# Performance work log

Measured on AMD Instinct MI355X. Metric: run time of the kernel, lower is better.

## Reference

```python
import jax, jax.numpy as jnp
import numpy as np

DIM = 1024
GROUP = 16
N_LIN = 18   # 6 blocks * 3 quantized linears
N_LN = 5
RANK = 32
BATCH = 32768


def _dequant(q, s):
    # q: [DIM, DIM] int values in [0,16); s: [DIM*DIM/GROUP] per-group scales
    w = (q.reshape(-1, GROUP).astype(jnp.float32) - 8.0) * s[:, None]
    return w.reshape(DIM, DIM)


def _qlora_linear(x, q, s, b, la, lb):
    # x: [N, DIM]; la: [RANK, DIM]; lb: [DIM, RANK]
    w = _dequant(q, s)
    base = x @ w.T + b
    lora = (x @ la.T) @ lb.T
    return base + lora


def _layernorm(x, g, b):
    m = jnp.mean(x, axis=-1, keepdims=True)
    v = jnp.var(x, axis=-1, keepdims=True)
    return (x - m) / jnp.sqrt(v + 1e-5) * g + b


def setup_inputs() -> dict:
    key = jax.random.key(0)
    ks = jax.random.split(key, 8)
    x = jax.random.normal(ks[0], (BATCH, DIM), dtype=jnp.float32)
    wq = jax.random.randint(ks[1], (N_LIN, DIM, DIM), 0, 16, dtype=jnp.int32)
    scales = jax.random.uniform(ks[2], (N_LIN, DIM * DIM // GROUP), dtype=jnp.float32) * 0.02 + 1e-3
    bias = jax.random.normal(ks[3], (N_LIN, DIM), dtype=jnp.float32) * 0.02
    lora_a = jax.random.normal(ks[4], (N_LIN, RANK, DIM), dtype=jnp.float32) * 0.05
    lora_b = jax.random.normal(ks[5], (N_LIN, DIM, RANK), dtype=jnp.float32) * 0.05
    gamma = jnp.ones((N_LN, DIM), dtype=jnp.float32)
    beta = jnp.zeros((N_LN, DIM), dtype=jnp.float32)
    return {"x": x, "wq": wq, "scales": scales, "bias": bias,
            "lora_a": lora_a, "lora_b": lora_b, "gamma": gamma, "beta": beta}


def reference(x, wq, scales, bias, lora_a, lora_b, gamma, beta):
    h = x.astype(jnp.float32)
    li = 0
    for blk in range(6):
        r = h
        for j in range(3):
            h = _qlora_linear(h, wq[li], scales[li], bias[li], lora_a[li], lora_b[li])
            li += 1
            if j < 2:
                h = jax.nn.relu(h)
        h = h + r
        if blk < 5:
            h = _layernorm(h, gamma[blk], beta[blk])
    return h
```

## Files before the change

kernel.cpp:

```cpp
#include <hip/hip_runtime.h>

typedef unsigned int u32;
typedef unsigned short u16;
typedef _Float16 f16;
typedef f16 f16x8 __attribute__((ext_vector_type(8)));
typedef float f32x4 __attribute__((ext_vector_type(4)));
typedef u16 u16x8 __attribute__((ext_vector_type(8)));

#define DIM 1024
#define BATCH 32768
#define RANK 32
#define NLIN 18

__device__ __forceinline__ u16 f2h(float f) {
    f16 h = (f16)f;
    return *(u16*)&h;
}
__device__ __forceinline__ float h2f(u16 u) {
    f16 h;
    *(u16*)&h = u;
    return (float)h;
}

__device__ __forceinline__ void gload16(const u16* g, u16* l) {
    __builtin_amdgcn_global_load_lds((__attribute__((address_space(1))) const void*)g,
                                     (__attribute__((address_space(3))) void*)l,
                                     16, 0, 0);
}

#define BAR()        __builtin_amdgcn_s_barrier()
#define SB0()        __builtin_amdgcn_sched_barrier(0)
#define ASM_VM0()    asm volatile("s_waitcnt vmcnt(0)" ::: "memory")
#define ASM_VM4()    asm volatile("s_waitcnt vmcnt(4)" ::: "memory")
#define ASM_VM8()    asm volatile("s_waitcnt vmcnt(8)" ::: "memory")
#define ASM_LG0()    asm volatile("s_waitcnt lgkmcnt(0)" ::: "memory")
#define ASM_LG4()    asm volatile("s_waitcnt lgkmcnt(4)" ::: "memory")

__global__ __launch_bounds__(256) void build_weff(
    const int* __restrict__ wq, const float* __restrict__ scales,
    const float* __restrict__ la, const float* __restrict__ lb,
    u16* __restrict__ weff)
{
    const int rb = blockIdx.x;
    const int li = blockIdx.y;
    const int tid = threadIdx.x;
    const int row0 = rb * 16;
    const int* wqL = wq + (size_t)li * DIM * DIM;
    const float* sL = scales + (size_t)li * (DIM * DIM / 16);
    const float* laL = la + (size_t)li * RANK * DIM;
    const float* lbL = lb + (size_t)li * DIM * RANK;
    u16* wout = weff + (size_t)li * DIM * DIM;

    for (int kc = 0; kc < 4; ++kc) {
        const int k = kc * 256 + tid;
        float lar[RANK];
        #pragma unroll
        for (int r = 0; r < RANK; ++r) lar[r] = laL[r * DIM + k];
        const int ks = k >> 4;
        #pragma unroll
        for (int og = 0; og < 16; og += 4) {
            const int m0 = row0 + og;
            float a0 = ((float)wqL[(m0 + 0) * DIM + k] - 8.0f) * sL[((m0 + 0) << 6) + ks];
            float a1 = ((float)wqL[(m0 + 1) * DIM + k] - 8.0f) * sL[((m0 + 1) << 6) + ks];
            float a2 = ((float)wqL[(m0 + 2) * DIM + k] - 8.0f) * sL[((m0 + 2) << 6) + ks];
            float a3 = ((float)wqL[(m0 + 3) * DIM + k] - 8.0f) * sL[((m0 + 3) << 6) + ks];
            #pragma unroll
            for (int r = 0; r < RANK; ++r) {
                const float lv = lar[r];
                a0 += lbL[(m0 + 0) * RANK + r] * lv;
                a1 += lbL[(m0 + 1) * RANK + r] * lv;
                a2 += lbL[(m0 + 2) * RANK + r] * lv;
                a3 += lbL[(m0 + 3) * RANK + r] * lv;
            }
            wout[(m0 + 0) * DIM + k] = f2h(a0);
            wout[(m0 + 1) * DIM + k] = f2h(a1);
            wout[(m0 + 2) * DIM + k] = f2h(a2);
            wout[(m0 + 3) * DIM + k] = f2h(a3);
        }
    }
}

__global__ __launch_bounds__(256) void xcast(const float* __restrict__ x, u16* __restrict__ o) {
    size_t i = ((size_t)blockIdx.x * 256 + threadIdx.x) * 8;
    float4 a = *(const float4*)(x + i);
    float4 b = *(const float4*)(x + i + 4);
    u16x8 v;
    v[0] = f2h(a.x); v[1] = f2h(a.y); v[2] = f2h(a.z); v[3] = f2h(a.w);
    v[4] = f2h(b.x); v[5] = f2h(b.y); v[6] = f2h(b.z); v[7] = f2h(b.w);
    *(u16x8*)(o + i) = v;
}

template<int EPI>
__global__ __launch_bounds__(512, 2) void gemm256(
    const u16* __restrict__ X, const u16* __restrict__ W,
    const float* __restrict__ bias, const u16* __restrict__ res,
    void* __restrict__ outp)
{
    __shared__ __align__(16) u16 As3[3 * 16384];
    __shared__ __align__(16) u16 Bs[2 * 16384];
    const int tid = threadIdx.x;
    const int bid = blockIdx.x;
    const int wg = (bid & 7) * 64 + (bid >> 3);
    const int bm = wg >> 2;
    const int bn = wg & 3;
    const int wid = tid >> 6;
    const int lane = tid & 63;
    const int wm = wid >> 2;
    const int wn = wid & 3;

    const int c1 = tid, c2 = tid + 512;
    const int r1 = c1 >> 3, r2 = c2 >> 3;
    const int l1 = ((c1 & 7) ^ (r1 & 7)) * 8;
    const int l2 = ((c2 & 7) ^ (r2 & 7)) * 8;
    const u16* gA0a = X + (size_t)(bm * 256 +       r1) * DIM + l1;
    const u16* gA0b = X + (size_t)(bm * 256 +       r2) * DIM + l2;
    const u16* gA1a = X + (size_t)(bm * 256 + 128 + r1) * DIM + l1;
    const u16* gA1b = X + (size_t)(bm * 256 + 128 + r2) * DIM + l2;
    const u16* gB0a = W + (size_t)(bn * 256 +       r1) * DIM + l1;
    const u16* gB0b = W + (size_t)(bn * 256 +       r2) * DIM + l2;
    const u16* gB1a = W + (size_t)(bn * 256 + 128 + r1) * DIM + l1;
    const u16* gB1b = W + (size_t)(bn * 256 + 128 + r2) * DIM + l2;
    const int d1 = c1 * 8, d2 = c2 * 8;

    const int kg = lane >> 4;
    const int sw = lane & 7;
    const int ch0 = ((0 * 4 + kg) ^ sw) * 8;
    const int ch1 = ((1 * 4 + kg) ^ sw) * 8;
    const int aoff = (wm * 128 + (lane & 15)) * 64;
    const int boff = (wn * 64 + (lane & 15)) * 64;

    f32x4 acc[8][4];
    #pragma unroll
    for (int i = 0; i < 8; ++i)
        #pragma unroll
        for (int j = 0; j < 4; ++j)
            acc[i][j] = (f32x4){0.f, 0.f, 0.f, 0.f};
    f16x8 af[4][2];
    f16x8 bf[4][2];

    #define RD_A(MH, BUF) { \
        _Pragma("unroll") \
        for (int fm = 0; fm < 4; ++fm) { \
            af[fm][0] = *(const f16x8*)&(BUF)[aoff + ((MH)*64 + fm*16)*64 + ch0]; \
            af[fm][1] = *(const f16x8*)&(BUF)[aoff + ((MH)*64 + fm*16)*64 + ch1]; \
        } }
    #define RD_B01(BUF) { \
        _Pragma("unroll") \
        for (int fn = 0; fn < 2; ++fn) { \
            bf[fn][0] = *(const f16x8*)&(BUF)[boff + (fn*16)*64 + ch0]; \
            bf[fn][1] = *(const f16x8*)&(BUF)[boff + (fn*16)*64 + ch1]; \
        } }
    #define RD_B23(BUF) { \
        _Pragma("unroll") \
        for (int fn = 2; fn < 4; ++fn) { \
            bf[fn][0] = *(const f16x8*)&(BUF)[boff + (fn*16)*64 + ch0]; \
            bf[fn][1] = *(const f16x8*)&(BUF)[boff + (fn*16)*64 + ch1]; \
        } }
    #define QUAD(MH, NH) { \
        __builtin_amdgcn_s_setprio(1); \
        _Pragma("unroll") \
        for (int ks = 0; ks < 2; ++ks) \
            _Pragma("unroll") \
            for (int fm = 0; fm < 4; ++fm) \
                _Pragma("unroll") \
                for (int fn = 0; fn < 2; ++fn) \
                    acc[(MH)*4+fm][(NH)*2+fn] = __builtin_amdgcn_mfma_f32_16x16x32_f16( \
                        af[fm][ks], bf[(NH)*2+fn][ks], acc[(MH)*4+fm][(NH)*2+fn], 0, 0, 0); \
        __builtin_amdgcn_s_setprio(0); }

    gload16(gA0a, &As3[d1]);        gload16(gA0b, &As3[d2]);
    gload16(gA1a, &As3[8192 + d1]); gload16(gA1b, &As3[8192 + d2]);
    gload16(gB0a, &Bs[d1]);         gload16(gB0b, &Bs[d2]);
    gload16(gB1a, &Bs[8192 + d1]);  gload16(gB1b, &Bs[8192 + d2]);
    gload16(gA0a + 64, &As3[16384 + d1]);        gload16(gA0b + 64, &As3[16384 + d2]);
    gload16(gA1a + 64, &As3[16384 + 8192 + d1]); gload16(gA1b + 64, &As3[16384 + 8192 + d2]);
    gload16(gB0a + 64, &Bs[16384 + d1]);         gload16(gB0b + 64, &Bs[16384 + d2]);
    gload16(gB1a + 64, &Bs[16384 + 8192 + d1]);  gload16(gB1b + 64, &Bs[16384 + 8192 + d2]);

    ASM_VM8();
    BAR();
    RD_A(0, (&As3[0]));
    RD_B01((&Bs[0]));
    SB0();

    int aCur = 0, aNext = 16384, aWr = 32768;
    #pragma unroll 1
    for (int t = 0; t < 16; ++t) {
        const int ko2 = (t + 2) * 64;
        const bool st = (t <= 13);
        const int bCur = (t & 1) ? 16384 : 0;
        const int bNext = bCur ^ 16384;
        RD_B23((&Bs[bCur]));
        if (st) { gload16(gA0a + ko2, &As3[aWr + d1]); gload16(gA0b + ko2, &As3[aWr + d2]);
                  gload16(gA1a + ko2, &As3[aWr + 8192 + d1]); gload16(gA1b + ko2, &As3[aWr + 8192 + d2]); }
        SB0();
        BAR();
        ASM_LG4(); SB0();
        QUAD(0, 0);
        BAR();
        ASM_LG0(); SB0();
        QUAD(0, 1);
        RD_A(1, (&As3[aCur]));
        SB0();
        if (st) ASM_VM4(); else if (t == 14) ASM_VM0();
        BAR();
        ASM_LG0(); SB0();
        QUAD(1, 0);
        if (t <= 14) RD_B01((&Bs[bNext]));
        if (st) { gload16(gB0a + ko2, &Bs[bCur + d1]); gload16(gB0b + ko2, &Bs[bCur + d2]);
                  gload16(gB1a + ko2, &Bs[bCur + 8192 + d1]); gload16(gB1b + ko2, &Bs[bCur + 8192 + d2]); }
        SB0();
        BAR();
        SB0();
        QUAD(1, 1);
        if (t <= 14) RD_A(0, (&As3[aNext]));
        SB0();
        int tmp = aCur; aCur = aNext; aNext = aWr; aWr = tmp;
    }

    ASM_LG0();
    float* blk = (float*)&As3[0] + wid * 1088;
    const int mrow = bm * 256 + wm * 128;
    const int ncol = bn * 256 + wn * 64 + (lane & 7) * 8;
    float4 bv0 = *(const float4*)&bias[ncol];
    float4 bv1 = *(const float4*)&bias[ncol + 4];
    u16x8 rvp[2][2];
    if (EPI != 0) {
        #pragma unroll
        for (int pass = 0; pass < 2; ++pass) {
            const int m = mrow + pass * 8 + (lane >> 3);
            rvp[0][pass] = *(const u16x8*)(res + (size_t)m * DIM + ncol);
        }
    }
    #pragma unroll
    for (int fm = 0; fm < 8; ++fm) {
        if (EPI != 0 && fm < 7) {
            #pragma unroll
            for (int pass = 0; pass < 2; ++pass) {
                const int m = mrow + (fm + 1) * 16 + pass * 8 + (lane >> 3);
                rvp[(fm + 1) & 1][pass] = *(const u16x8*)(res + (size_t)m * DIM + ncol);
            }
        }
        __builtin_amdgcn_sched_barrier(0);
        #pragma unroll
        for (int fn = 0; fn < 4; ++fn)
            #pragma unroll
            for (int reg = 0; reg < 4; ++reg)
                blk[((lane >> 4) * 4 + reg) * 68 + (lane & 15) + fn * 16] = acc[fm][fn][reg];
        ASM_LG0();
        __builtin_amdgcn_sched_barrier(0);
        #pragma unroll
        for (int pass = 0; pass < 2; ++pass) {
            const float* rp = &blk[(pass * 8 + (lane >> 3)) * 68 + (lane & 7) * 8];
            float4 v0 = *(const float4*)rp;
            float4 v1 = *(const float4*)(rp + 4);
            v0.x += bv0.x; v0.y += bv0.y; v0.z += bv0.z; v0.w += bv0.w;
            v1.x += bv1.x; v1.y += bv1.y; v1.z += bv1.z; v1.w += bv1.w;
            const int m = mrow + fm * 16 + pass * 8 + (lane >> 3);
            const size_t gi = (size_t)m * DIM + ncol;
            if (EPI == 0) {
                u16x8 o;
                o[0] = f2h(fmaxf(v0.x, 0.f)); o[1] = f2h(fmaxf(v0.y, 0.f));
                o[2] = f2h(fmaxf(v0.z, 0.f)); o[3] = f2h(fmaxf(v0.w, 0.f));
                o[4] = f2h(fmaxf(v1.x, 0.f)); o[5] = f2h(fmaxf(v1.y, 0.f));
                o[6] = f2h(fmaxf(v1.z, 0.f)); o[7] = f2h(fmaxf(v1.w, 0.f));
                *(u16x8*)((u16*)outp + gi) = o;
            } else {
                u16x8 rv = rvp[fm & 1][pass];
                v0.x += h2f(rv[0]); v0.y += h2f(rv[1]); v0.z += h2f(rv[2]); v0.w += h2f(rv[3]);
                v1.x += h2f(rv[4]); v1.y += h2f(rv[5]); v1.z += h2f(rv[6]); v1.w += h2f(rv[7]);
                if (EPI == 1) {
                    u16x8 o;
                    o[0] = f2h(v0.x); o[1] = f2h(v0.y); o[2] = f2h(v0.z); o[3] = f2h(v0.w);
                    o[4] = f2h(v1.x); o[5] = f2h(v1.y); o[6] = f2h(v1.z); o[7] = f2h(v1.w);
                    *(u16x8*)((u16*)outp + gi) = o;
                } else {
                    *(float4*)((float*)outp + gi) = v0;
                    *(float4*)((float*)outp + gi + 4) = v1;
                }
            }
        }
        ASM_LG0();
    }
    #undef RD_A
    #undef RD_B01
    #undef RD_B23
    #undef QUAD
}

__global__ __launch_bounds__(256) void ln_k(const u16* __restrict__ in,
    const float* __restrict__ g, const float* __restrict__ b, u16* __restrict__ out)
{
    int row = blockIdx.x * 4 + (threadIdx.x >> 6);
    int lane = threadIdx.x & 63;
    const u16* rp = in + (size_t)row * DIM;
    u16x8 v0 = *(const u16x8*)(rp + lane * 8);
    u16x8 v1 = *(const u16x8*)(rp + 512 + lane * 8);
    float f[16];
    #pragma unroll
    for (int j = 0; j < 8; ++j) { f[j] = h2f(v0[j]); f[8 + j] = h2f(v1[j]); }
    float s = 0.f, sq = 0.f;
    #pragma unroll
    for (int j = 0; j < 16; ++j) { s += f[j]; sq += f[j] * f[j]; }
    #pragma unroll
    for (int m = 1; m < 64; m <<= 1) { s += __shfl_xor(s, m); sq += __shfl_xor(sq, m); }
    float mean = s * (1.0f / 1024.0f);
    float var = sq * (1.0f / 1024.0f) - mean * mean;
    float rstd = 1.0f / sqrtf(var + 1e-5f);
    u16x8 o0, o1;
    #pragma unroll
    for (int j = 0; j < 8; ++j) {
        int c0 = lane * 8 + j, c1 = 512 + lane * 8 + j;
        o0[j] = f2h((f[j] - mean) * rstd * g[c0] + b[c0]);
        o1[j] = f2h((f[8 + j] - mean) * rstd * g[c1] + b[c1]);
    }
    u16* op = out + (size_t)row * DIM;
    *(u16x8*)(op + lane * 8) = o0;
    *(u16x8*)(op + 512 + lane * 8) = o1;
}

extern "C" void kernel_launch(void* const* d_in, const int* in_sizes, int n_in,
                              void* d_out, int out_size, void* d_ws, size_t ws_size,
                              hipStream_t stream) {
    const float* x      = (const float*)d_in[0];
    const int*   wq     = (const int*)d_in[1];
    const float* scales = (const float*)d_in[2];
    const float* bias   = (const float*)d_in[3];
    const float* la     = (const float*)d_in[4];
    const float* lb     = (const float*)d_in[5];
    const float* gamma  = (const float*)d_in[6];
    const float* beta   = (const float*)d_in[7];

    char* ws = (char*)d_ws;
    u16* Weff = (u16*)ws;
    u16* actA = (u16*)(ws + (size_t)NLIN * DIM * DIM * 2);
    u16* actB = actA + (size_t)BATCH * DIM;
    u16* dob  = (u16*)d_out;
    float* dof = (float*)d_out;

    build_weff<<<dim3(64, 18), 256, 0, stream>>>(wq, scales, la, lb, Weff);
    xcast<<<(BATCH * DIM) / 2048, 256, 0, stream>>>(x, actA);

    int li = 0;
    for (int blk = 0; blk < 6; ++blk) {
        const u16* w0 = Weff + (size_t)(li + 0) * DIM * DIM;
        const u16* w1 = Weff + (size_t)(li + 1) * DIM * DIM;
        const u16* w2 = Weff + (size_t)(li + 2) * DIM * DIM;
        const float* b0 = bias + (li + 0) * DIM;
        const float* b1 = bias + (li + 1) * DIM;
        const float* b2 = bias + (li + 2) * DIM;
        if (blk < 5) {
            gemm256<0><<<512, 512, 0, stream>>>(actA, w0, b0, nullptr, actB);
            gemm256<0><<<512, 512, 0, stream>>>(actB, w1, b1, nullptr, dob);
            gemm256<1><<<512, 512, 0, stream>>>(dob,  w2, b2, actA, actB);
            ln_k<<<BATCH / 4, 256, 0, stream>>>(actB, gamma + blk * DIM, beta + blk * DIM, actA);
        } else {
            gemm256<0><<<512, 512, 0, stream>>>(actA, w0, b0, nullptr, dob);
            gemm256<0><<<512, 512, 0, stream>>>(dob,  w1, b1, nullptr, actB);
            gemm256<2><<<512, 512, 0, stream>>>(actB, w2, b2, actA, (void*)dof);
        }
        li += 3;
    }
}
```

Baseline: 1.462 ms.

## Replace 256x256 GEMM tile with 128x128 tile, 32-wide k-steps, triple buffering

The 512-thread 256x256 GEMM is replaced by a 256-thread kernel computing 128x128 output tiles with K step 32 and three-stage LDS buffering for both A and B. Shared memory moves to a k-group-major layout without XOR swizzle, the grid grows from 512 to 2048 blocks, and launch bounds target 3 blocks per CU. The aim is better occupancy and latency hiding with a simpler pipeline. In exchange, arithmetic intensity per tile drops, global/L2 traffic rises, and there are twice as many barriers per K.

```diff
diff --git a/kernel.cpp b/kernel.cpp
--- a/kernel.cpp
+++ b/kernel.cpp
@@ -32,9 +32,7 @@
 #define SB0()        __builtin_amdgcn_sched_barrier(0)
 #define ASM_VM0()    asm volatile("s_waitcnt vmcnt(0)" ::: "memory")
 #define ASM_VM4()    asm volatile("s_waitcnt vmcnt(4)" ::: "memory")
-#define ASM_VM8()    asm volatile("s_waitcnt vmcnt(8)" ::: "memory")
 #define ASM_LG0()    asm volatile("s_waitcnt lgkmcnt(0)" ::: "memory")
-#define ASM_LG4()    asm volatile("s_waitcnt lgkmcnt(4)" ::: "memory")
 
 __global__ __launch_bounds__(256) void build_weff(
     const int* __restrict__ wq, const float* __restrict__ scales,
@@ -91,137 +89,92 @@
 }
 
 template<int EPI>
-__global__ __launch_bounds__(512, 2) void gemm256(
+__global__ __launch_bounds__(256, 3) void gemm128(
     const u16* __restrict__ X, const u16* __restrict__ W,
     const float* __restrict__ bias, const u16* __restrict__ res,
     void* __restrict__ outp)
 {
-    __shared__ __align__(16) u16 As3[3 * 16384];
-    __shared__ __align__(16) u16 Bs[2 * 16384];
+    __shared__ __align__(16) u16 As3[3 * 4096];
+    __shared__ __align__(16) u16 Bs3[3 * 4096];
     const int tid = threadIdx.x;
     const int bid = blockIdx.x;
-    const int wg = (bid & 7) * 64 + (bid >> 3);
-    const int bm = wg >> 2;
-    const int bn = wg & 3;
+    const int wg = (bid & 7) * 256 + (bid >> 3);
+    const int bm = wg >> 3;
+    const int bn = wg & 7;
     const int wid = tid >> 6;
     const int lane = tid & 63;
-    const int wm = wid >> 2;
-    const int wn = wid & 3;
-
-    const int c1 = tid, c2 = tid + 512;
-    const int r1 = c1 >> 3, r2 = c2 >> 3;
-    const int l1 = ((c1 & 7) ^ (r1 & 7)) * 8;
-    const int l2 = ((c2 & 7) ^ (r2 & 7)) * 8;
-    const u16* gA0a = X + (size_t)(bm * 256 +       r1) * DIM + l1;
-    const u16* gA0b = X + (size_t)(bm * 256 +       r2) * DIM + l2;
-    const u16* gA1a = X + (size_t)(bm * 256 + 128 + r1) * DIM + l1;
-    const u16* gA1b = X + (size_t)(bm * 256 + 128 + r2) * DIM + l2;
-    const u16* gB0a = W + (size_t)(bn * 256 +       r1) * DIM + l1;
-    const u16* gB0b = W + (size_t)(bn * 256 +       r2) * DIM + l2;
-    const u16* gB1a = W + (size_t)(bn * 256 + 128 + r1) * DIM + l1;
-    const u16* gB1b = W + (size_t)(bn * 256 + 128 + r2) * DIM + l2;
-    const int d1 = c1 * 8, d2 = c2 * 8;
+    const int wm = wid >> 1;
+    const int wn = wid & 1;
+
+    const int srow = tid & 127;
+    const int skg = tid >> 7;
+    const u16* gA = X + (size_t)(bm * 128 + srow) * DIM + skg * 8;
+    const u16* gB = W + (size_t)(bn * 128 + srow) * DIM + skg * 8;
+    const int d1 = tid * 8;
 
     const int kg = lane >> 4;
-    const int sw = lane & 7;
-    const int ch0 = ((0 * 4 + kg) ^ sw) * 8;
-    const int ch1 = ((1 * 4 + kg) ^ sw) * 8;
-    const int aoff = (wm * 128 + (lane & 15)) * 64;
-    const int boff = (wn * 64 + (lane & 15)) * 64;
-
-    f32x4 acc[8][4];
-    #pragma unroll
-    for (int i = 0; i < 8; ++i)
+    const int r16 = lane & 15;
+    const int aBase = kg * 1024 + (wm * 64 + r16) * 8;
+    const int bBase = kg * 1024 + (wn * 64 + r16) * 8;
+
+    f32x4 acc[4][4];
+    #pragma unroll
+    for (int i = 0; i < 4; ++i)
         #pragma unroll
         for (int j = 0; j < 4; ++j)
             acc[i][j] = (f32x4){0.f, 0.f, 0.f, 0.f};
-    f16x8 af[4][2];
-    f16x8 bf[4][2];
-
-    #define RD_A(MH, BUF) { \
+    f16x8 af[4], bf[4];
+
+    #define STAGE(KT, OFF) { \
+        const u16* ga_ = gA + (KT) * 32; \
+        const u16* gb_ = gB + (KT) * 32; \
+        gload16(ga_,      &As3[(OFF) + d1]); \
+        gload16(ga_ + 16, &As3[(OFF) + d1 + 2048]); \
+        gload16(gb_,      &Bs3[(OFF) + d1]); \
+        gload16(gb_ + 16, &Bs3[(OFF) + d1 + 2048]); }
+    #define RD_FRAGS(OFF) { \
         _Pragma("unroll") \
-        for (int fm = 0; fm < 4; ++fm) { \
-            af[fm][0] = *(const f16x8*)&(BUF)[aoff + ((MH)*64 + fm*16)*64 + ch0]; \
-            af[fm][1] = *(const f16x8*)&(BUF)[aoff + ((MH)*64 + fm*16)*64 + ch1]; \
+        for (int f = 0; f < 4; ++f) { \
+            af[f] = *(const f16x8*)&As3[(OFF) + aBase + f * 128]; \
+            bf[f] = *(const f16x8*)&Bs3[(OFF) + bBase + f * 128]; \
         } }
-    #define RD_B01(BUF) { \
-        _Pragma("unroll") \
-        for (int fn = 0; fn < 2; ++fn) { \
-            bf[fn][0] = *(const f16x8*)&(BUF)[boff + (fn*16)*64 + ch0]; \
-            bf[fn][1] = *(const f16x8*)&(BUF)[boff + (fn*16)*64 + ch1]; \
-        } }
-    #define RD_B23(BUF) { \
-        _Pragma("unroll") \
-        for (int fn = 2; fn < 4; ++fn) { \
-            bf[fn][0] = *(const f16x8*)&(BUF)[boff + (fn*16)*64 + ch0]; \
-            bf[fn][1] = *(const f16x8*)&(BUF)[boff + (fn*16)*64 + ch1]; \
-        } }
-    #define QUAD(MH, NH) { \
+    #define QUADS() { \
         __builtin_amdgcn_s_setprio(1); \
         _Pragma("unroll") \
-        for (int ks = 0; ks < 2; ++ks) \
+        for (int m = 0; m < 4; ++m) \
             _Pragma("unroll") \
-            for (int fm = 0; fm < 4; ++fm) \
-                _Pragma("unroll") \
-                for (int fn = 0; fn < 2; ++fn) \
-                    acc[(MH)*4+fm][(NH)*2+fn] = __builtin_amdgcn_mfma_f32_16x16x32_f16( \
-                        af[fm][ks], bf[(NH)*2+fn][ks], acc[(MH)*4+fm][(NH)*2+fn], 0, 0, 0); \
+            for (int n = 0; n < 4; ++n) \
+                acc[m][n] = __builtin_amdgcn_mfma_f32_16x16x32_f16( \
+                    af[m], bf[n], acc[m][n], 0, 0, 0); \
         __builtin_amdgcn_s_setprio(0); }
 
-    gload16(gA0a, &As3[d1]);        gload16(gA0b, &As3[d2]);
-    gload16(gA1a, &As3[8192 + d1]); gload16(gA1b, &As3[8192 + d2]);
-    gload16(gB0a, &Bs[d1]);         gload16(gB0b, &Bs[d2]);
-    gload16(gB1a, &Bs[8192 + d1]);  gload16(gB1b, &Bs[8192 + d2]);
-    gload16(gA0a + 64, &As3[16384 + d1]);        gload16(gA0b + 64, &As3[16384 + d2]);
-    gload16(gA1a + 64, &As3[16384 + 8192 + d1]); gload16(gA1b + 64, &As3[16384 + 8192 + d2]);
-    gload16(gB0a + 64, &Bs[16384 + d1]);         gload16(gB0b + 64, &Bs[16384 + d2]);
-    gload16(gB1a + 64, &Bs[16384 + 8192 + d1]);  gload16(gB1b + 64, &Bs[16384 + 8192 + d2]);
-
-    ASM_VM8();
+    STAGE(0, 0);
+    STAGE(1, 4096);
+    ASM_VM4();
     BAR();
-    RD_A(0, (&As3[0]));
-    RD_B01((&Bs[0]));
+    RD_FRAGS(0);
     SB0();
 
-    int aCur = 0, aNext = 16384, aWr = 32768;
+    int oCur = 0, oNext = 4096, oWr = 8192;
     #pragma unroll 1
-    for (int t = 0; t < 16; ++t) {
-        const int ko2 = (t + 2) * 64;
-        const bool st = (t <= 13);
-        const int bCur = (t & 1) ? 16384 : 0;
-        const int bNext = bCur ^ 16384;
-        RD_B23((&Bs[bCur]));
-        if (st) { gload16(gA0a + ko2, &As3[aWr + d1]); gload16(gA0b + ko2, &As3[aWr + d2]);
-                  gload16(gA1a + ko2, &As3[aWr + 8192 + d1]); gload16(gA1b + ko2, &As3[aWr + 8192 + d2]); }
-        SB0();
+    for (int t = 0; t < 32; ++t) {
         BAR();
-        ASM_LG4(); SB0();
-        QUAD(0, 0);
+        if (t <= 29) STAGE(t + 2, oWr);
+        if (t <= 29) ASM_VM4();
+        else if (t == 30) ASM_VM0();
         BAR();
         ASM_LG0(); SB0();
-        QUAD(0, 1);
-        RD_A(1, (&As3[aCur]));
+        QUADS();
+        if (t <= 30) RD_FRAGS(oNext);
         SB0();
-        if (st) ASM_VM4(); else if (t == 14) ASM_VM0();
-        BAR();
-        ASM_LG0(); SB0();
-        QUAD(1, 0);
-        if (t <= 14) RD_B01((&Bs[bNext]));
-        if (st) { gload16(gB0a + ko2, &Bs[bCur + d1]); gload16(gB0b + ko2, &Bs[bCur + d2]);
-                  gload16(gB1a + ko2, &Bs[bCur + 8192 + d1]); gload16(gB1b + ko2, &Bs[bCur + 8192 + d2]); }
-        SB0();
-        BAR();
-        SB0();
-        QUAD(1, 1);
-        if (t <= 14) RD_A(0, (&As3[aNext]));
-        SB0();
-        int tmp = aCur; aCur = aNext; aNext = aWr; aWr = tmp;
+        int tmp = oCur; oCur = oNext; oNext = oWr; oWr = tmp;
     }
 
     ASM_LG0();
+    BAR();
     float* blk = (float*)&As3[0] + wid * 1088;
-    const int mrow = bm * 256 + wm * 128;
-    const int ncol = bn * 256 + wn * 64 + (lane & 7) * 8;
+    const int mrow = bm * 128 + wm * 64;
+    const int ncol = bn * 128 + wn * 64 + (lane & 7) * 8;
     float4 bv0 = *(const float4*)&bias[ncol];
     float4 bv1 = *(const float4*)&bias[ncol + 4];
     u16x8 rvp[2][2];
@@ -233,8 +186,8 @@
         }
     }
     #pragma unroll
-    for (int fm = 0; fm < 8; ++fm) {
-        if (EPI != 0 && fm < 7) {
+    for (int fm = 0; fm < 4; ++fm) {
+        if (EPI != 0 && fm < 3) {
             #pragma unroll
             for (int pass = 0; pass < 2; ++pass) {
                 const int m = mrow + (fm + 1) * 16 + pass * 8 + (lane >> 3);
@@ -282,10 +235,9 @@
         }
         ASM_LG0();
     }
-    #undef RD_A
-    #undef RD_B01
-    #undef RD_B23
-    #undef QUAD
+    #undef STAGE
+    #undef RD_FRAGS
+    #undef QUADS
 }
 
 __global__ __launch_bounds__(256) void ln_k(const u16* __restrict__ in,
@@ -350,14 +302,14 @@
         const float* b1 = bias + (li + 1) * DIM;
         const float* b2 = bias + (li + 2) * DIM;
         if (blk < 5) {
-            gemm256<0><<<512, 512, 0, stream>>>(actA, w0, b0, nullptr, actB);
-            gemm256<0><<<512, 512, 0, stream>>>(actB, w1, b1, nullptr, dob);
-            gemm256<1><<<512, 512, 0, stream>>>(dob,  w2, b2, actA, actB);
+            gemm128<0><<<2048, 256, 0, stream>>>(actA, w0, b0, nullptr, actB);
+            gemm128<0><<<2048, 256, 0, stream>>>(actB, w1, b1, nullptr, dob);
+            gemm128<1><<<2048, 256, 0, stream>>>(dob,  w2, b2, actA, actB);
             ln_k<<<BATCH / 4, 256, 0, stream>>>(actB, gamma + blk * DIM, beta + blk * DIM, actA);
         } else {
-            gemm256<0><<<512, 512, 0, stream>>>(actA, w0, b0, nullptr, dob);
-            gemm256<0><<<512, 512, 0, stream>>>(dob,  w1, b1, nullptr, actB);
-            gemm256<2><<<512, 512, 0, stream>>>(actB, w2, b2, actA, (void*)dof);
+            gemm128<0><<<2048, 256, 0, stream>>>(actA, w0, b0, nullptr, dob);
+            gemm128<0><<<2048, 256, 0, stream>>>(dob,  w1, b1, nullptr, actB);
+            gemm128<2><<<2048, 256, 0, stream>>>(actB, w2, b2, actA, (void*)dof);
         }
         li += 3;
     }
```

Result: slower. 2.578 ms (+76.3%).
